# Kernel tuning notes

Measured on AMD Instinct MI355X. Metric: run time of the kernel, lower is better.

## Reference

```python
import jax, jax.numpy as jnp
import numpy as np

N_NODES = 100000
N_EDGES = 640000
D_IN = 128
D_OUT = 128

def setup_inputs() -> dict:
    key = jax.random.key(0)
    k1, k2, k3, k4, k5 = jax.random.split(key, 5)
    feat = jax.random.normal(k1, (N_NODES, D_IN), dtype=jnp.float32)
    src = jax.random.randint(k2, (N_EDGES,), 0, N_NODES, dtype=jnp.int32)
    dst = jax.random.randint(k3, (N_EDGES,), 0, N_NODES, dtype=jnp.int32)
    scale = 1.0 / np.sqrt(D_IN)
    W_self = jax.random.normal(k4, (D_IN, D_OUT), dtype=jnp.float32) * scale
    W_neigh = jax.random.normal(k5, (D_IN, D_OUT), dtype=jnp.float32) * scale
    b_self = jnp.zeros((D_OUT,), dtype=jnp.float32)
    b_neigh = jnp.zeros((D_OUT,), dtype=jnp.float32)
    return {"feat": feat, "src": src, "dst": dst,
            "W_self": W_self, "b_self": b_self,
            "W_neigh": W_neigh, "b_neigh": b_neigh}

def reference(feat, src, dst, W_self, b_self, W_neigh, b_neigh):
    # GraphSAGE 'mean' aggregator: copy_src + mean reduce over in-edges, then
    # rst = fc_self(h_self) + fc_neigh(h_neigh). feat_drop=0, no activation/norm.
    n = feat.shape[0]
    msg = feat[src]                                   # [E, D_in] gather
    neigh_sum = jax.ops.segment_sum(msg, dst, num_segments=n)      # [N, D_in]
    deg = jax.ops.segment_sum(jnp.ones_like(dst, dtype=feat.dtype), dst,
                              num_segments=n)          # [N]
    # mean with zero-in-degree nodes -> 0 (DGL semantics)
    h_neigh = neigh_sum / jnp.maximum(deg, 1.0)[:, None]
    rst = feat @ W_self + b_self + h_neigh @ W_neigh + b_neigh      # [N, D_out]
    return rst
```

## Files before the change

kernel.cpp:

```cpp
#include <hip/hip_runtime.h>


constexpr int N_NODES = 100000;
constexpr int N_EDGES = 640000;
constexpr int D = 128;

constexpr int SCAN_ELEMS_PER_BLOCK = 1024;
constexpr int SCAN_NBLOCKS = (N_NODES + SCAN_ELEMS_PER_BLOCK - 1) / SCAN_ELEMS_PER_BLOCK;

typedef __attribute__((ext_vector_type(8))) short bf16x8;
typedef __attribute__((ext_vector_type(4))) float f32x4;

__device__ __forceinline__ unsigned short f2bf(float f) {
    unsigned int u = __float_as_uint(f);
    unsigned int r = u + 0x7FFFu + ((u >> 16) & 1u);
    return (unsigned short)(r >> 16);
}

__global__ __launch_bounds__(256) void zero_deg_kernel(int4* __restrict__ deg4) {
    int i = blockIdx.x * 256 + threadIdx.x;
    if (i < N_NODES / 4) deg4[i] = int4{0, 0, 0, 0};
}

__global__ void prepass_kernel(const int* __restrict__ dst, int* __restrict__ deg,
                               const float* __restrict__ Ws, const float* __restrict__ Wn,
                               unsigned short* __restrict__ wp,
                               const float* __restrict__ feat, unsigned short* __restrict__ fb) {
    const int gid = blockIdx.x * blockDim.x + threadIdx.x;
    if (gid < N_EDGES) atomicAdd(&deg[dst[gid]], 1);
    if (gid < 2 * D * D) {
        int i = gid;
        int r  = i & 7;
        int c  = (i >> 3) & 127;
        int h  = (i >> 10) & 3;
        int ks = (i >> 12) & 3;
        int m  = i >> 14;
        const float* W = m ? Wn : Ws;
        int k = ks * 32 + h * 8 + r;
        wp[i] = f2bf(W[k * D + c]);
    }
    const int total4 = N_NODES * D / 4;
    for (int i = gid; i < total4; i += N_EDGES) {
        float4 v = ((const float4*)feat)[i];
        ushort4 o;
        o.x = f2bf(v.x); o.y = f2bf(v.y); o.z = f2bf(v.z); o.w = f2bf(v.w);
        ((ushort4*)fb)[i] = o;
    }
}


__global__ __launch_bounds__(256) void partial_kernel(const int* __restrict__ deg,
                                                      int* __restrict__ bsum) {
    __shared__ int wsum[4];
    const int tid = threadIdx.x;
    const int base = (blockIdx.x * 256 + tid) * 4;
    int s = 0;
    #pragma unroll
    for (int j = 0; j < 4; j++) {
        int idx = base + j;
        if (idx < N_NODES) s += deg[idx];
    }
    for (int off = 32; off > 0; off >>= 1) s += __shfl_down(s, off, 64);
    if ((tid & 63) == 0) wsum[tid >> 6] = s;
    __syncthreads();
    if (tid == 0) bsum[blockIdx.x] = wsum[0] + wsum[1] + wsum[2] + wsum[3];
}

__global__ __launch_bounds__(128) void scanb_kernel(const int* __restrict__ bsum,
                                                    int* __restrict__ boff,
                                                    int* __restrict__ rowptr) {
    __shared__ int s[128];
    const int tid = threadIdx.x;
    int v = (tid < SCAN_NBLOCKS) ? bsum[tid] : 0;
    s[tid] = v;
    __syncthreads();
    for (int off = 1; off < 128; off <<= 1) {
        int u = (tid >= off) ? s[tid - off] : 0;
        __syncthreads();
        s[tid] += u;
        __syncthreads();
    }
    if (tid < SCAN_NBLOCKS) boff[tid] = s[tid] - v;
    if (tid == 0) rowptr[N_NODES] = N_EDGES;
}

__global__ __launch_bounds__(256) void final_kernel(const int* __restrict__ deg,
                                                    const int* __restrict__ boff,
                                                    int* __restrict__ rowptr,
                                                    int* __restrict__ cursor) {
    __shared__ int wsum[4];
    const int tid = threadIdx.x;
    const int lane = tid & 63;
    const int wave = tid >> 6;
    const int base = (blockIdx.x * 256 + tid) * 4;

    int local[4];
    int tsum = 0;
    #pragma unroll
    for (int j = 0; j < 4; j++) {
        int idx = base + j;
        local[j] = (idx < N_NODES) ? deg[idx] : 0;
        tsum += local[j];
    }
    int incl = tsum;
    for (int off = 1; off < 64; off <<= 1) {
        int u = __shfl_up(incl, off, 64);
        if (lane >= off) incl += u;
    }
    if (lane == 63) wsum[wave] = incl;
    __syncthreads();
    int woff = 0;
    for (int w = 0; w < 4; w++) woff += (w < wave) ? wsum[w] : 0;

    int run = boff[blockIdx.x] + woff + (incl - tsum);
    #pragma unroll
    for (int j = 0; j < 4; j++) {
        int idx = base + j;
        if (idx < N_NODES) {
            rowptr[idx] = run;
            cursor[idx] = run;
            run += local[j];
        }
    }
}

__global__ void fill_kernel(const int* __restrict__ src, const int* __restrict__ dst,
                            int* __restrict__ cursor, int* __restrict__ csr_src) {
    int e = blockIdx.x * blockDim.x + threadIdx.x;
    if (e < N_EDGES) {
        int pos = atomicAdd(&cursor[dst[e]], 1);
        csr_src[pos] = src[e];
    }
}

__global__ __launch_bounds__(256) void gather_kernel(
    const unsigned short* __restrict__ fb, const int* __restrict__ csr_src,
    const int* __restrict__ rowptr, unsigned short* __restrict__ hn)
{
    const int lane = threadIdx.x & 63;
    const int n = (blockIdx.x * blockDim.x + threadIdx.x) >> 6;
    if (n >= N_NODES) return;

    const int e0 = rowptr[n];
    const int e1 = rowptr[n + 1];

    float ax = 0.f, ay = 0.f;
    for (int base = e0; base < e1; base += 8) {
        int sidx[8];
        #pragma unroll
        for (int j = 0; j < 8; j++) {
            int ee = base + j;
            ee = (ee < e1) ? ee : (e1 - 1);
            sidx[j] = csr_src[ee];
        }
        unsigned int v[8];
        #pragma unroll
        for (int j = 0; j < 8; j++)
            v[j] = ((const unsigned int*)(fb + (size_t)sidx[j] * D))[lane];
        #pragma unroll
        for (int j = 0; j < 8; j++) {
            const float w = (base + j < e1) ? 1.0f : 0.0f;
            ax = fmaf(w, __uint_as_float(v[j] << 16), ax);
            ay = fmaf(w, __uint_as_float(v[j] & 0xFFFF0000u), ay);
        }
    }
    const float sc = 1.0f / (float)max(e1 - e0, 1);
    const unsigned int packed =
        ((unsigned int)f2bf(ay * sc) << 16) | (unsigned int)f2bf(ax * sc);
    ((unsigned int*)(hn + (size_t)n * D))[lane] = packed;
}

__global__ __launch_bounds__(256) void mmfused_kernel(
    const unsigned short* __restrict__ fb, const unsigned short* __restrict__ hn,
    const unsigned short* __restrict__ wp,
    const float* __restrict__ b_self, const float* __restrict__ b_neigh,
    float* __restrict__ out)
{
    __shared__ unsigned short lw[2 * 4 * 4 * 128 * 8];

    const int tid = threadIdx.x;
    {
        const uint4* s = (const uint4*)wp;
        uint4* d = (uint4*)lw;
        #pragma unroll
        for (int i = 0; i < 16; i++) d[tid + i * 256] = s[tid + i * 256];
    }
    __syncthreads();

    const int wave = tid >> 6, lane = tid & 63;
    const int h = lane >> 4, c = lane & 15;
    const int row_base = blockIdx.x * 128 + wave * 32;

    bf16x8 a[2][2][4];
    #pragma unroll
    for (int ti = 0; ti < 2; ti++) {
        int row = row_base + ti * 16 + c;
        int rowc = min(row, N_NODES - 1);
        const bf16x8* f0 = (const bf16x8*)(fb + (size_t)rowc * D);
        const bf16x8* f1 = (const bf16x8*)(hn + (size_t)rowc * D);
        #pragma unroll
        for (int ks = 0; ks < 4; ks++) {
            a[0][ti][ks] = f0[ks * 4 + h];
            a[1][ti][ks] = f1[ks * 4 + h];
        }
    }

    for (int ct = 0; ct < 8; ct++) {
        f32x4 acc[2];
        #pragma unroll
        for (int ti = 0; ti < 2; ti++) acc[ti] = f32x4{0.f, 0.f, 0.f, 0.f};

        #pragma unroll
        for (int m = 0; m < 2; m++) {
            bf16x8 b[4];
            #pragma unroll
            for (int ks = 0; ks < 4; ks++)
                b[ks] = ((const bf16x8*)lw)[((m * 4 + ks) * 4 + h) * 128 + ct * 16 + c];
            #pragma unroll
            for (int ks = 0; ks < 4; ks++)
                #pragma unroll
                for (int ti = 0; ti < 2; ti++)
                    acc[ti] = __builtin_amdgcn_mfma_f32_16x16x32_bf16(a[m][ti][ks], b[ks], acc[ti], 0, 0, 0);
        }

        const int col = ct * 16 + c;
        const float bias = b_self[col] + b_neigh[col];
        #pragma unroll
        for (int ti = 0; ti < 2; ti++) {
            if (row_base + ti * 16 < N_NODES) {
                #pragma unroll
                for (int q = 0; q < 4; q++) {
                    int row = row_base + ti * 16 + h * 4 + q;
                    out[(size_t)row * D + col] = acc[ti][q] + bias;
                }
            }
        }
    }
}

extern "C" void kernel_launch(void* const* d_in, const int* in_sizes, int n_in,
                              void* d_out, int out_size, void* d_ws, size_t ws_size,
                              hipStream_t stream) {
    const float* feat    = (const float*)d_in[0];
    const int*   src     = (const int*)d_in[1];
    const int*   dst     = (const int*)d_in[2];
    const float* W_self  = (const float*)d_in[3];
    const float* b_self  = (const float*)d_in[4];
    const float* W_neigh = (const float*)d_in[5];
    const float* b_neigh = (const float*)d_in[6];
    float* out = (float*)d_out;

    unsigned short* fb = (unsigned short*)d_ws;
    unsigned short* hn = fb + (size_t)N_NODES * D;
    unsigned short* wp = hn + (size_t)N_NODES * D;
    int*   deg     = (int*)(wp + 2 * D * D);
    int*   rowptr  = deg + N_NODES;
    int*   cursor  = rowptr + (N_NODES + 1);
    int*   csr_src = cursor + N_NODES;
    int*   bsum    = csr_src + N_EDGES;
    int*   boff    = bsum + SCAN_NBLOCKS;

    zero_deg_kernel<<<(N_NODES / 4 + 255) / 256, 256, 0, stream>>>((int4*)deg);

    prepass_kernel<<<(N_EDGES + 255) / 256, 256, 0, stream>>>(dst, deg, W_self, W_neigh,
                                                              wp, feat, fb);

    partial_kernel<<<SCAN_NBLOCKS, 256, 0, stream>>>(deg, bsum);
    scanb_kernel<<<1, 128, 0, stream>>>(bsum, boff, rowptr);
    final_kernel<<<SCAN_NBLOCKS, 256, 0, stream>>>(deg, boff, rowptr, cursor);

    fill_kernel<<<(N_EDGES + 255) / 256, 256, 0, stream>>>(src, dst, cursor, csr_src);

    gather_kernel<<<25000, 256, 0, stream>>>(fb, csr_src, rowptr, hn);

    mmfused_kernel<<<(N_NODES + 127) / 128, 256, 0, stream>>>(fb, hn, wp, b_self, b_neigh, out);
}
```

Before: 137.3 us.

## Merge scan kernels with grid barrier, read weights from global, nontemporal stores

```diff
diff --git a/kernel.cpp b/kernel.cpp
--- a/kernel.cpp
+++ b/kernel.cpp
@@ -5,8 +5,7 @@
 constexpr int N_EDGES = 640000;
 constexpr int D = 128;
 
-constexpr int SCAN_ELEMS_PER_BLOCK = 1024;
-constexpr int SCAN_NBLOCKS = (N_NODES + SCAN_ELEMS_PER_BLOCK - 1) / SCAN_ELEMS_PER_BLOCK;
+constexpr int SCAN_NBLOCKS = 98;
 
 typedef __attribute__((ext_vector_type(8))) short bf16x8;
 typedef __attribute__((ext_vector_type(4))) float f32x4;
@@ -25,8 +24,10 @@
 __global__ void prepass_kernel(const int* __restrict__ dst, int* __restrict__ deg,
                                const float* __restrict__ Ws, const float* __restrict__ Wn,
                                unsigned short* __restrict__ wp,
-                               const float* __restrict__ feat, unsigned short* __restrict__ fb) {
+                               const float* __restrict__ feat, unsigned short* __restrict__ fb,
+                               int* __restrict__ ctr) {
     const int gid = blockIdx.x * blockDim.x + threadIdx.x;
+    if (gid == 0) ctr[0] = 0;
     if (gid < N_EDGES) atomicAdd(&deg[dst[gid]], 1);
     if (gid < 2 * D * D) {
         int i = gid;
@@ -48,46 +49,11 @@
     }
 }
 
-
-__global__ __launch_bounds__(256) void partial_kernel(const int* __restrict__ deg,
-                                                      int* __restrict__ bsum) {
-    __shared__ int wsum[4];
-    const int tid = threadIdx.x;
-    const int base = (blockIdx.x * 256 + tid) * 4;
-    int s = 0;
-    #pragma unroll
-    for (int j = 0; j < 4; j++) {
-        int idx = base + j;
-        if (idx < N_NODES) s += deg[idx];
-    }
-    for (int off = 32; off > 0; off >>= 1) s += __shfl_down(s, off, 64);
-    if ((tid & 63) == 0) wsum[tid >> 6] = s;
-    __syncthreads();
-    if (tid == 0) bsum[blockIdx.x] = wsum[0] + wsum[1] + wsum[2] + wsum[3];
-}
-
-__global__ __launch_bounds__(128) void scanb_kernel(const int* __restrict__ bsum,
-                                                    int* __restrict__ boff,
-                                                    int* __restrict__ rowptr) {
-    __shared__ int s[128];
-    const int tid = threadIdx.x;
-    int v = (tid < SCAN_NBLOCKS) ? bsum[tid] : 0;
-    s[tid] = v;
-    __syncthreads();
-    for (int off = 1; off < 128; off <<= 1) {
-        int u = (tid >= off) ? s[tid - off] : 0;
-        __syncthreads();
-        s[tid] += u;
-        __syncthreads();
-    }
-    if (tid < SCAN_NBLOCKS) boff[tid] = s[tid] - v;
-    if (tid == 0) rowptr[N_NODES] = N_EDGES;
-}
-
-__global__ __launch_bounds__(256) void final_kernel(const int* __restrict__ deg,
-                                                    const int* __restrict__ boff,
-                                                    int* __restrict__ rowptr,
-                                                    int* __restrict__ cursor) {
+__global__ __launch_bounds__(256) void scan_kernel(const int* __restrict__ deg,
+                                                   int* __restrict__ rowptr,
+                                                   int* __restrict__ cursor,
+                                                   int* __restrict__ bsum,
+                                                   int* __restrict__ ctr) {
     __shared__ int wsum[4];
     const int tid = threadIdx.x;
     const int lane = tid & 63;
@@ -102,6 +68,29 @@
         local[j] = (idx < N_NODES) ? deg[idx] : 0;
         tsum += local[j];
     }
+    {
+        int s = tsum;
+        for (int off = 32; off > 0; off >>= 1) s += __shfl_down(s, off, 64);
+        if (lane == 0) wsum[wave] = s;
+        __syncthreads();
+        if (tid == 0) bsum[blockIdx.x] = wsum[0] + wsum[1] + wsum[2] + wsum[3];
+    }
+    __syncthreads();
+    if (tid == 0) {
+        __threadfence();
+        __hip_atomic_fetch_add(ctr, 1, __ATOMIC_ACQ_REL, __HIP_MEMORY_SCOPE_AGENT);
+        while (__hip_atomic_load(ctr, __ATOMIC_ACQUIRE, __HIP_MEMORY_SCOPE_AGENT)
+               < SCAN_NBLOCKS) {}
+    }
+    __syncthreads();
+
+    int v = (tid < blockIdx.x) ? bsum[tid] : 0;
+    for (int off = 32; off > 0; off >>= 1) v += __shfl_down(v, off, 64);
+    if (lane == 0) wsum[wave] = v;
+    __syncthreads();
+    const int boff = wsum[0] + wsum[1] + wsum[2] + wsum[3];
+    __syncthreads();
+
     int incl = tsum;
     for (int off = 1; off < 64; off <<= 1) {
         int u = __shfl_up(incl, off, 64);
@@ -112,7 +101,7 @@
     int woff = 0;
     for (int w = 0; w < 4; w++) woff += (w < wave) ? wsum[w] : 0;
 
-    int run = boff[blockIdx.x] + woff + (incl - tsum);
+    int run = boff + woff + (incl - tsum);
     #pragma unroll
     for (int j = 0; j < 4; j++) {
         int idx = base + j;
@@ -122,6 +111,7 @@
             run += local[j];
         }
     }
+    if (blockIdx.x == 0 && tid == 0) rowptr[N_NODES] = N_EDGES;
 }
 
 __global__ void fill_kernel(const int* __restrict__ src, const int* __restrict__ dst,
@@ -176,17 +166,7 @@
     const float* __restrict__ b_self, const float* __restrict__ b_neigh,
     float* __restrict__ out)
 {
-    __shared__ unsigned short lw[2 * 4 * 4 * 128 * 8];
-
     const int tid = threadIdx.x;
-    {
-        const uint4* s = (const uint4*)wp;
-        uint4* d = (uint4*)lw;
-        #pragma unroll
-        for (int i = 0; i < 16; i++) d[tid + i * 256] = s[tid + i * 256];
-    }
-    __syncthreads();
-
     const int wave = tid >> 6, lane = tid & 63;
     const int h = lane >> 4, c = lane & 15;
     const int row_base = blockIdx.x * 128 + wave * 32;
@@ -205,6 +185,7 @@
         }
     }
 
+    const bf16x8* wpv = (const bf16x8*)wp;
     for (int ct = 0; ct < 8; ct++) {
         f32x4 acc[2];
         #pragma unroll
@@ -215,7 +196,7 @@
             bf16x8 b[4];
             #pragma unroll
             for (int ks = 0; ks < 4; ks++)
-                b[ks] = ((const bf16x8*)lw)[((m * 4 + ks) * 4 + h) * 128 + ct * 16 + c];
+                b[ks] = wpv[((m * 4 + ks) * 4 + h) * 128 + ct * 16 + c];
             #pragma unroll
             for (int ks = 0; ks < 4; ks++)
                 #pragma unroll
@@ -231,7 +212,8 @@
                 #pragma unroll
                 for (int q = 0; q < 4; q++) {
                     int row = row_base + ti * 16 + h * 4 + q;
-                    out[(size_t)row * D + col] = acc[ti][q] + bias;
+                    __builtin_nontemporal_store(acc[ti][q] + bias,
+                                                &out[(size_t)row * D + col]);
                 }
             }
         }
@@ -258,16 +240,14 @@
     int*   cursor  = rowptr + (N_NODES + 1);
     int*   csr_src = cursor + N_NODES;
     int*   bsum    = csr_src + N_EDGES;
-    int*   boff    = bsum + SCAN_NBLOCKS;
+    int*   ctr     = bsum + SCAN_NBLOCKS;
 
     zero_deg_kernel<<<(N_NODES / 4 + 255) / 256, 256, 0, stream>>>((int4*)deg);
 
     prepass_kernel<<<(N_EDGES + 255) / 256, 256, 0, stream>>>(dst, deg, W_self, W_neigh,
-                                                              wp, feat, fb);
-
-    partial_kernel<<<SCAN_NBLOCKS, 256, 0, stream>>>(deg, bsum);
-    scanb_kernel<<<1, 128, 0, stream>>>(bsum, boff, rowptr);
-    final_kernel<<<SCAN_NBLOCKS, 256, 0, stream>>>(deg, boff, rowptr, cursor);
+                                                              wp, feat, fb, ctr);
+
+    scan_kernel<<<SCAN_NBLOCKS, 256, 0, stream>>>(deg, rowptr, cursor, bsum, ctr);
 
     fill_kernel<<<(N_EDGES + 255) / 256, 256, 0, stream>>>(src, dst, cursor, csr_src);
 
```

Result: no change. 139.1 us (+1.3%).
